# Kernel optimization log

Hardware: AMD Instinct MI355X
Metric: run time of the kernel (lower is better)

## Reference

```python
import math
import jax, jax.numpy as jnp
import numpy as np

N_HEAD = 16
N_KV_HEAD = 4
HEAD_DIM = 64
EPS = 1e-6  # flax nnx.RMSNorm default epsilon
NEG_INF = -1000000000.0


def apply_rotary_emb(x, cos, sin):
    # x: (B,T,H,hd); cos/sin broadcast to (B,T,H,hd//2)
    d = x.shape[3] // 2
    x1, x2 = x[..., :d], x[..., d:]
    y1 = x1 * cos + x2 * sin
    y2 = x1 * -sin + x2 * cos
    return jnp.concatenate([y1, y2], axis=3).astype(x.dtype)


def rmsnorm_noscale(x):
    # flax nnx.RMSNorm(use_scale=False): x * rsqrt(mean(x^2) + eps)
    ms = jnp.mean(jnp.square(x), axis=-1, keepdims=True)
    return x * jax.lax.rsqrt(ms + EPS)


def setup_inputs() -> dict:
    key = jax.random.key(0)
    ks = jax.random.split(key, 7)
    B, T, C = 2, 2048, 1024
    sc = 1.0 / math.sqrt(C)
    x = jax.random.normal(ks[0], (B, T, C), jnp.float32)
    # realistic rotary tables
    pos = jnp.arange(T, dtype=jnp.float32)
    inv_freq = 1.0 / (10000.0 ** (jnp.arange(0, HEAD_DIM // 2, dtype=jnp.float32) / (HEAD_DIM // 2)))
    ang = pos[:, None] * inv_freq[None, :]  # (T, hd/2)
    cos = jnp.cos(ang)[None, :, None, :]
    sin = jnp.sin(ang)[None, :, None, :]
    Wq = jax.random.normal(ks[1], (C, N_HEAD * HEAD_DIM), jnp.float32) * sc
    Wk = jax.random.normal(ks[2], (C, N_KV_HEAD * HEAD_DIM), jnp.float32) * sc
    Wv = jax.random.normal(ks[3], (C, N_KV_HEAD * HEAD_DIM), jnp.float32) * sc
    Wo = jax.random.normal(ks[4], (C, C), jnp.float32) * sc
    return {"x": x, "cos": cos, "sin": sin, "Wq": Wq, "Wk": Wk, "Wv": Wv, "Wo": Wo}


def reference(x, cos, sin, Wq, Wk, Wv, Wo):
    B, T, C = x.shape
    q = (x @ Wq).reshape(B, T, N_HEAD, HEAD_DIM)
    k = (x @ Wk).reshape(B, T, N_KV_HEAD, HEAD_DIM)
    v = (x @ Wv).reshape(B, T, N_KV_HEAD, HEAD_DIM)
    q = rmsnorm_noscale(apply_rotary_emb(q, cos, sin))
    k = rmsnorm_noscale(apply_rotary_emb(k, cos, sin))
    q = jnp.transpose(q, (0, 2, 1, 3))  # (B,H,T,hd)
    k = jnp.transpose(k, (0, 2, 1, 3))  # (B,KV,T,hd)
    v = jnp.transpose(v, (0, 2, 1, 3))
    n_rep = N_HEAD // N_KV_HEAD
    k = jnp.repeat(k, n_rep, axis=1)
    v = jnp.repeat(v, n_rep, axis=1)
    scale = 1.0 / math.sqrt(HEAD_DIM)
    logits = jnp.einsum('bhtd,bhsd->bhts', q, k) * scale
    causal = jnp.where(jnp.tril(jnp.ones((T, T), dtype=jnp.bool_)), 0.0, NEG_INF)
    logits = logits + causal
    w = jax.nn.softmax(logits, axis=-1)
    y = jnp.einsum('bhts,bhsd->bhtd', w, v)
    y = jnp.transpose(y, (0, 2, 1, 3)).reshape(B, T, C)
    return y @ Wo
```

## Files before the change

kernel.cpp:

```cpp
#include <hip/hip_runtime.h>
#include <hip/hip_bf16.h>
#include <math.h>

#define EPS 1e-6f
#define LOG2E 1.44269504088896340736f

typedef __attribute__((ext_vector_type(8))) short short8;
typedef __attribute__((ext_vector_type(4))) short short4v;
typedef __attribute__((ext_vector_type(4))) float f32x4;

static __device__ __forceinline__ short f2bf(float x) {
    unsigned u = __builtin_bit_cast(unsigned, x);
    u += 0x7fffu + ((u >> 16) & 1u);
    return (short)(u >> 16);
}
static __device__ __forceinline__ float bf2f(short s) {
    unsigned u = ((unsigned)(unsigned short)s) << 16;
    return __builtin_bit_cast(float, u);
}

typedef __attribute__((address_space(1))) const void gvoid_t;
typedef __attribute__((address_space(3))) void lvoid_t;
static __device__ __forceinline__ void gload_lds16(const void* g, void* l) {
    __builtin_amdgcn_global_load_lds((gvoid_t*)g, (lvoid_t*)l, 16, 0, 0);
}

__global__ __launch_bounds__(256) void prep_inputs(
    const float* __restrict__ x, const float* __restrict__ Wq,
    const float* __restrict__ Wk, const float* __restrict__ Wv,
    const float* __restrict__ Wo, short* __restrict__ x16,
    short* __restrict__ WT, short* __restrict__ WoT, int n8) {
    if ((int)blockIdx.x < 2048) {
        const int i = blockIdx.x * 256 + threadIdx.x;
        if (i >= n8) return;
        const float4 a = reinterpret_cast<const float4*>(x)[2 * i];
        const float4 b = reinterpret_cast<const float4*>(x)[2 * i + 1];
        short8 o;
        o[0] = f2bf(a.x); o[1] = f2bf(a.y); o[2] = f2bf(a.z); o[3] = f2bf(a.w);
        o[4] = f2bf(b.x); o[5] = f2bf(b.y); o[6] = f2bf(b.z); o[7] = f2bf(b.w);
        reinterpret_cast<short8*>(x16)[i] = o;
        return;
    }
    __shared__ short tl[64][65];
    int t = blockIdx.x - 2048;
    const float* src; short* dst; int N, nx;
    if (t < 256)      { src = Wq; dst = WT;                N = 1024; nx = 16; }
    else if (t < 320) { src = Wk; dst = WT + 1024 * 1024;  N = 256;  nx = 4;  t -= 256; }
    else if (t < 384) { src = Wv; dst = WT + 1280 * 1024;  N = 256;  nx = 4;  t -= 320; }
    else              { src = Wo; dst = WoT;               N = 1024; nx = 16; t -= 384; }
    const int n0 = (t % nx) * 64, k0 = (t / nx) * 64;
    const int tid = threadIdx.x;

    #pragma unroll
    for (int i = 0; i < 4; ++i) {
        const int kr = (tid >> 4) + i * 16;
        const int c4 = (tid & 15) * 4;
        const float4 v = *reinterpret_cast<const float4*>(
            &src[(size_t)(k0 + kr) * N + n0 + c4]);
        tl[kr][c4 + 0] = f2bf(v.x);
        tl[kr][c4 + 1] = f2bf(v.y);
        tl[kr][c4 + 2] = f2bf(v.z);
        tl[kr][c4 + 3] = f2bf(v.w);
    }
    __syncthreads();

    const int nr  = tid >> 2;
    const int kc0 = (tid & 3) * 16;
    short tmp[16];
    #pragma unroll
    for (int j = 0; j < 16; ++j) tmp[j] = tl[kc0 + j][nr];
    short8* outp = reinterpret_cast<short8*>(&dst[(size_t)(n0 + nr) * 1024 + k0 + kc0]);
    outp[0] = *reinterpret_cast<short8*>(&tmp[0]);
    outp[1] = *reinterpret_cast<short8*>(&tmp[8]);
}

template <int OB>
__global__ __launch_bounds__(256) void gemm_bf16(const short* __restrict__ A,
                                                 const short* __restrict__ BT,
                                                 float* __restrict__ Cf,
                                                 short* __restrict__ Cb,
                                                 int M, int N, int K) {
    __shared__ short As[2][128 * 64];
    __shared__ short Bs[2][64 * 64];

    const int tid  = threadIdx.x;
    const int lane = tid & 63;
    const int w    = tid >> 6;
    const int lq = lane & 15, lh = lane >> 4;
    const int wm = w >> 1,   wn = w & 1;
    const size_t arow0 = (size_t)blockIdx.x * 128;
    const size_t brow0 = (size_t)blockIdx.y * 64;

    const int sr  = lane >> 3;
    const int sc  = lane & 7;
    const int scg = sc ^ sr;

    f32x4 acc[4][2];
    #pragma unroll
    for (int mi = 0; mi < 4; ++mi)
        #pragma unroll
        for (int ni = 0; ni < 2; ++ni) acc[mi][ni] = (f32x4){0.f, 0.f, 0.f, 0.f};

    const int NT = K >> 6;

    auto STAGE = [&](int u, int k0) {
        #pragma unroll
        for (int i = 0; i < 4; ++i) {
            const int rg = w * 4 + i;
            gload_lds16(A + (arow0 + rg * 8 + sr) * K + k0 + scg * 8,
                        &As[u][rg * 8 * 64]);
        }
        #pragma unroll
        for (int i = 0; i < 2; ++i) {
            const int rg = w * 2 + i;
            gload_lds16(BT + (brow0 + rg * 8 + sr) * K + k0 + scg * 8,
                        &Bs[u][rg * 8 * 64]);
        }
    };

    STAGE(0, 0);
    __syncthreads();
    int cur = 0;

    for (int t = 0; t < NT; ++t) {
        if (t + 1 < NT) STAGE(cur ^ 1, (t + 1) << 6);

        #pragma unroll
        for (int dk = 0; dk < 2; ++dk) {
            short8 af[4], bf[2];
            #pragma unroll
            for (int mi = 0; mi < 4; ++mi) {
                const int r = wm * 64 + mi * 16 + lq;
                af[mi] = *reinterpret_cast<const short8*>(
                    &As[cur][r * 64 + (((dk * 4 + lh) ^ (lq & 7)) * 8)]);
            }
            #pragma unroll
            for (int ni = 0; ni < 2; ++ni) {
                const int r = wn * 32 + ni * 16 + lq;
                bf[ni] = *reinterpret_cast<const short8*>(
                    &Bs[cur][r * 64 + (((dk * 4 + lh) ^ (lq & 7)) * 8)]);
            }
            __builtin_amdgcn_s_setprio(1);
            #pragma unroll
            for (int mi = 0; mi < 4; ++mi)
                #pragma unroll
                for (int ni = 0; ni < 2; ++ni)
                    acc[mi][ni] = __builtin_amdgcn_mfma_f32_16x16x32_bf16(
                        af[mi], bf[ni], acc[mi][ni], 0, 0, 0);
            __builtin_amdgcn_s_setprio(0);
        }

        __syncthreads();
        cur ^= 1;
    }

    #pragma unroll
    for (int mi = 0; mi < 4; ++mi) {
        const size_t row = arow0 + wm * 64 + mi * 16 + lh * 4;
        #pragma unroll
        for (int ni = 0; ni < 2; ++ni) {
            const size_t col = brow0 + wn * 32 + ni * 16 + lq;
            #pragma unroll
            for (int i = 0; i < 4; ++i) {
                if (OB) Cb[(row + i) * N + col] = f2bf(acc[mi][ni][i]);
                else    Cf[(row + i) * N + col] = acc[mi][ni][i];
            }
        }
    }
}

__global__ __launch_bounds__(256) void rope_v_prep(
    const short* __restrict__ qkv16, const float* __restrict__ cosb,
    const float* __restrict__ sinb, short* __restrict__ q16,
    short* __restrict__ k16, short* __restrict__ vT, int B, int T) {
    const int NR = B * T * 5;
    if ((int)blockIdx.x < NR) {
        const int lane = threadIdx.x & 63;
        const int wid  = threadIdx.x >> 6;
        const int row  = blockIdx.x * 4 + wid;
        const int bt = row / 20;
        const int h  = row % 20;
        const int b  = bt / T, t = bt % T;

        const short* src = (h < 16) ? qkv16 + (size_t)bt * 1536 + h * 64
                                    : qkv16 + (size_t)bt * 1536 + 1024 + (h - 16) * 64;

        const int j = lane & 31;
        const float x1 = bf2f(src[j]);
        const float x2 = bf2f(src[j + 32]);
        const float c = cosb[t * 32 + j];
        const float s = sinb[t * 32 + j];
        float y = (lane < 32) ? (x1 * c + x2 * s) : (x2 * c - x1 * s);

        float ss = y * y;
        #pragma unroll
        for (int m = 1; m < 64; m <<= 1) ss += __shfl_xor(ss, m);
        const float r = rsqrtf(ss * (1.0f / 64.0f) + EPS);

        if (h < 16)
            q16[((size_t)(b * 16 + h) * T + t) * 64 + lane] = f2bf(y * r * (0.125f * LOG2E));
        else
            k16[((size_t)(b * 4 + (h - 16)) * T + t) * 64 + lane] = f2bf(y * r);
        return;
    }

    __shared__ short tl[64][65];
    const int vt = blockIdx.x - NR;
    const int ntile = T >> 6;
    const int b   = vt / (4 * ntile);
    const int kvh = (vt / ntile) & 3;
    const int t0  = (vt % ntile) * 64;
    const int tid = threadIdx.x;

    #pragma unroll
    for (int i = 0; i < 4; ++i) {
        const int tr = (tid >> 4) + i * 16;
        const int d4 = (tid & 15) * 4;
        const short4v v4 = *reinterpret_cast<const short4v*>(
            &qkv16[(size_t)(b * T + t0 + tr) * 1536 + 1280 + kvh * 64 + d4]);
        tl[tr][d4 + 0] = v4[0];
        tl[tr][d4 + 1] = v4[1];
        tl[tr][d4 + 2] = v4[2];
        tl[tr][d4 + 3] = v4[3];
    }
    __syncthreads();

    const int dim = tid >> 2;
    const int tq  = (tid & 3) * 16;
    const int hi  = (tq >> 4) & 1;
    const int a32 = tq & 32;
    short tmp[16];
    #pragma unroll
    for (int j2 = 0; j2 < 16; ++j2) tmp[j2] = tl[tq + j2][dim];
    short* orow = &vT[((size_t)(b * 4 + kvh) * 64 + dim) * T + t0];
    #pragma unroll
    for (int g = 0; g < 4; ++g) {
        *reinterpret_cast<short4v*>(orow + a32 + g * 8 + hi * 4) =
            *reinterpret_cast<short4v*>(&tmp[g * 4]);
    }
}

__global__ __launch_bounds__(128) void attn_mfma(
    const short* __restrict__ q16, const short* __restrict__ k16,
    const short* __restrict__ vT16, short* __restrict__ att16, int B, int T) {
    __shared__ short Kt[64 * 64];
    __shared__ short Vt[64 * 64];

    const int tid  = threadIdx.x;
    const int lane = tid & 63;
    const int w    = tid >> 6;
    const int lq   = lane & 15;
    const int lh   = lane >> 4;

    const int idx = blockIdx.x;
    const int g   = idx & 7;
    const int j   = idx >> 3;
    const int b   = g >> 2;
    const int hk  = g & 3;
    const int qs  = (T >> 5) - 1 - (j >> 2);
    const int h   = hk * 4 + (j & 3);
    const int t0w = qs * 32 + w * 16;
    const int nt  = (qs >> 1) + 1;
    const bool evenq = !(qs & 1);

    const short* qrow = q16 + ((size_t)(b * 16 + h) * T + t0w + lq) * 64;
    const short8 qf0 = *reinterpret_cast<const short8*>(qrow + lh * 8);
    const short8 qf1 = *reinterpret_cast<const short8*>(qrow + 32 + lh * 8);

    const short* kgbase = k16 + (size_t)(b * 4 + hk) * T * 64;
    const short* vgbase = vT16 + (size_t)(b * 4 + hk) * 64 * T;

    const int sr  = lane >> 3;
    const int sc  = lane & 7;
    const int scg = sc ^ sr;

    short8 ones;
    #pragma unroll
    for (int i = 0; i < 8; ++i) ones[i] = (short)0x3F80;

    f32x4 yacc[4];
    #pragma unroll
    for (int dt = 0; dt < 4; ++dt) yacc[dt] = (f32x4){0.f, 0.f, 0.f, 0.f};
    f32x4 lacc = (f32x4){0.f, 0.f, 0.f, 0.f};

    for (int ti = 0; ti < nt; ++ti) {
        const int s0 = ti * 64;
        const bool last = (ti == nt - 1);
        const int kmax = (last && evenq) ? 2 : 4;
        __syncthreads();
        #pragma unroll
        for (int p2 = 0; p2 < 4; ++p2) {
            const int r = w * 32 + p2 * 8 + sr;
            gload_lds16(kgbase + (size_t)(s0 + r) * 64 + scg * 8,
                        &Kt[(w * 32 + p2 * 8) * 64]);
            gload_lds16(vgbase + (size_t)r * T + s0 + scg * 8,
                        &Vt[(w * 32 + p2 * 8) * 64]);
        }
        __syncthreads();

        f32x4 st[4];
        __builtin_amdgcn_s_setprio(1);
        #pragma unroll
        for (int ks = 0; ks < 4; ++ks) if (ks < kmax) {
            f32x4 a1 = (f32x4){0.f, 0.f, 0.f, 0.f};
            #pragma unroll
            for (int dk = 0; dk < 2; ++dk) {
                const short8 kfr = *reinterpret_cast<const short8*>(
                    (char*)Kt + (ks * 16 + lq) * 128 +
                    (((dk * 4 + lh) ^ (lq & 7)) * 16));
                a1 = __builtin_amdgcn_mfma_f32_16x16x32_bf16(
                    kfr, dk ? qf1 : qf0, a1, 0, 0, 0);
            }
            st[ks] = a1;
        }
        __builtin_amdgcn_s_setprio(0);

        if (last) {
            const int rloc = (qs & 1) * 32 + w * 16 + lq;
            #pragma unroll
            for (int ks = 0; ks < 4; ++ks) if (ks < kmax)
                #pragma unroll
                for (int i2 = 0; i2 < 4; ++i2)
                    if (ks * 16 + lh * 4 + i2 > rloc)
                        st[ks][i2] = -1e30f;
        }

        union { short8 s8; __hip_bfloat162 h2[4]; } pf[2];
        #pragma unroll
        for (int ks2 = 0; ks2 < 2; ++ks2) if (ks2 * 2 < kmax) {
            #pragma unroll
            for (int ks = 2 * ks2; ks < 2 * ks2 + 2; ++ks)
                #pragma unroll
                for (int i2 = 0; i2 < 4; ++i2)
                    st[ks][i2] = exp2f(st[ks][i2]);
            pf[ks2].h2[0] = __float22bfloat162_rn(float2{st[2 * ks2][0], st[2 * ks2][1]});
            pf[ks2].h2[1] = __float22bfloat162_rn(float2{st[2 * ks2][2], st[2 * ks2][3]});
            pf[ks2].h2[2] = __float22bfloat162_rn(float2{st[2 * ks2 + 1][0], st[2 * ks2 + 1][1]});
            pf[ks2].h2[3] = __float22bfloat162_rn(float2{st[2 * ks2 + 1][2], st[2 * ks2 + 1][3]});
        }

        __builtin_amdgcn_s_setprio(1);
        #pragma unroll
        for (int ks2 = 0; ks2 < 2; ++ks2) if (ks2 * 2 < kmax)
            lacc = __builtin_amdgcn_mfma_f32_16x16x32_bf16(ones, pf[ks2].s8, lacc, 0, 0, 0);
        #pragma unroll
        for (int dt = 0; dt < 4; ++dt) {
            const int rb = (dt * 16 + lq) * 128;
            const int sw = lq & 7;
            #pragma unroll
            for (int ks2 = 0; ks2 < 2; ++ks2) if (ks2 * 2 < kmax) {
                const short8 vf = *reinterpret_cast<const short8*>(
                    (const char*)Vt + rb + (((ks2 * 4 + lh) ^ sw) * 16));
                yacc[dt] = __builtin_amdgcn_mfma_f32_16x16x32_bf16(
                    vf, pf[ks2].s8, yacc[dt], 0, 0, 0);
            }
        }
        __builtin_amdgcn_s_setprio(0);
    }

    const float inv = 1.f / lacc[0];
    short* orow = att16 + (((size_t)b * T + t0w + lq) * 16 + h) * 64;
    #pragma unroll
    for (int dt = 0; dt < 4; ++dt) {
        short4v o;
        o[0] = f2bf(yacc[dt][0] * inv);
        o[1] = f2bf(yacc[dt][1] * inv);
        o[2] = f2bf(yacc[dt][2] * inv);
        o[3] = f2bf(yacc[dt][3] * inv);
        *reinterpret_cast<short4v*>(orow + dt * 16 + lh * 4) = o;
    }
}

extern "C" void kernel_launch(void* const* d_in, const int* in_sizes, int n_in,
                              void* d_out, int out_size, void* d_ws, size_t ws_size,
                              hipStream_t stream) {
    const float* x    = (const float*)d_in[0];
    const float* cosb = (const float*)d_in[1];
    const float* sinb = (const float*)d_in[2];
    const float* Wq   = (const float*)d_in[3];
    const float* Wk   = (const float*)d_in[4];
    const float* Wv   = (const float*)d_in[5];
    const float* Wo   = (const float*)d_in[6];
    float* out = (float*)d_out;

    const int B = 2, T = 2048;
    const int M = B * T;
    const size_t MB = 1 << 20;

    char* wsb = (char*)d_ws;
    short* qkv16 = (short*)(wsb);
    short* att16 = (short*)(wsb);
    short* x16   = (short*)(wsb + 24 * MB);
    short* q16   = (short*)(wsb + 24 * MB);
    short* WT    = (short*)(wsb + 32 * MB);
    short* k16   = (short*)(wsb + 32 * MB);
    short* vT16  = (short*)(wsb + 34 * MB);
    short* WoT   = (short*)(wsb + 36 * MB);

    prep_inputs<<<2048 + 640, 256, 0, stream>>>(x, Wq, Wk, Wv, Wo,
                                                x16, WT, WoT, M * 1024 / 8);

    gemm_bf16<1><<<dim3(M / 128, 1536 / 64), 256, 0, stream>>>(
        x16, WT, nullptr, qkv16, M, 1536, 1024);

    rope_v_prep<<<B * T * 5 + (T / 64) * 4 * B, 256, 0, stream>>>(
        qkv16, cosb, sinb, q16, k16, vT16, B, T);

    attn_mfma<<<dim3((T / 32) * 16 * B), 128, 0, stream>>>(q16, k16, vT16, att16, B, T);

    gemm_bf16<0><<<dim3(M / 128, 1024 / 64), 256, 0, stream>>>(
        att16, WoT, out, nullptr, M, 1024, 1024);
}
```

Baseline: 113.2 us.

## Fuse RoPE, RMSNorm and V transpose into QKV GEMM epilogue

The separate rope_v_prep kernel is removed. The QKV projection GEMM now stages its fp32 accumulator tile in shared memory and, per 64-column head block, applies rotary embedding, RMSNorm and scaling for Q/K, or transposes V, then writes the attention-ready layouts directly. This drops a kernel launch and the bf16 qkv intermediate round trip through global memory, and Q/K are normalised from fp32 rather than from rounded bf16 values. In exchange the GEMM epilogue gets longer, with a serial 32-row loop per wave doing shuffle reductions. The shared buffers are merged into one array so the epilogue can reuse them, and the workspace layout is adjusted.

```diff
diff --git a/kernel.cpp b/kernel.cpp
--- a/kernel.cpp
+++ b/kernel.cpp
@@ -74,15 +74,14 @@
     outp[1] = *reinterpret_cast<short8*>(&tmp[8]);
 }
 
-template <int OB>
-__global__ __launch_bounds__(256) void gemm_bf16(const short* __restrict__ A,
-                                                 const short* __restrict__ BT,
-                                                 float* __restrict__ Cf,
-                                                 short* __restrict__ Cb,
-                                                 int M, int N, int K) {
-    __shared__ short As[2][128 * 64];
-    __shared__ short Bs[2][64 * 64];
-
+__global__ __launch_bounds__(256) void gemm_qkv_fused(
+    const short* __restrict__ A, const short* __restrict__ BT,
+    const float* __restrict__ cosb, const float* __restrict__ sinb,
+    short* __restrict__ q16, short* __restrict__ k16, short* __restrict__ vT,
+    int B, int T) {
+    __shared__ short smem[2][(128 + 64) * 64];
+
+    const int K = 1024;
     const int tid  = threadIdx.x;
     const int lane = tid & 63;
     const int w    = tid >> 6;
@@ -104,17 +103,19 @@
     const int NT = K >> 6;
 
     auto STAGE = [&](int u, int k0) {
+        short* As = smem[u];
+        short* Bs = smem[u] + 128 * 64;
         #pragma unroll
         for (int i = 0; i < 4; ++i) {
             const int rg = w * 4 + i;
             gload_lds16(A + (arow0 + rg * 8 + sr) * K + k0 + scg * 8,
-                        &As[u][rg * 8 * 64]);
+                        &As[rg * 8 * 64]);
         }
         #pragma unroll
         for (int i = 0; i < 2; ++i) {
             const int rg = w * 2 + i;
             gload_lds16(BT + (brow0 + rg * 8 + sr) * K + k0 + scg * 8,
-                        &Bs[u][rg * 8 * 64]);
+                        &Bs[rg * 8 * 64]);
         }
     };
 
@@ -124,6 +125,8 @@
 
     for (int t = 0; t < NT; ++t) {
         if (t + 1 < NT) STAGE(cur ^ 1, (t + 1) << 6);
+        const short* As = smem[cur];
+        const short* Bs = smem[cur] + 128 * 64;
 
         #pragma unroll
         for (int dk = 0; dk < 2; ++dk) {
@@ -132,13 +135,13 @@
             for (int mi = 0; mi < 4; ++mi) {
                 const int r = wm * 64 + mi * 16 + lq;
                 af[mi] = *reinterpret_cast<const short8*>(
-                    &As[cur][r * 64 + (((dk * 4 + lh) ^ (lq & 7)) * 8)]);
+                    &As[r * 64 + (((dk * 4 + lh) ^ (lq & 7)) * 8)]);
             }
             #pragma unroll
             for (int ni = 0; ni < 2; ++ni) {
                 const int r = wn * 32 + ni * 16 + lq;
                 bf[ni] = *reinterpret_cast<const short8*>(
-                    &Bs[cur][r * 64 + (((dk * 4 + lh) ^ (lq & 7)) * 8)]);
+                    &Bs[r * 64 + (((dk * 4 + lh) ^ (lq & 7)) * 8)]);
             }
             __builtin_amdgcn_s_setprio(1);
             #pragma unroll
@@ -154,6 +157,147 @@
         cur ^= 1;
     }
 
+    float* fl = (float*)smem;
+    #pragma unroll
+    for (int mi = 0; mi < 4; ++mi) {
+        const int row = wm * 64 + mi * 16 + lh * 4;
+        #pragma unroll
+        for (int ni = 0; ni < 2; ++ni) {
+            const int col = wn * 32 + ni * 16 + lq;
+            #pragma unroll
+            for (int i = 0; i < 4; ++i)
+                fl[(row + i) * 66 + col] = acc[mi][ni][i];
+        }
+    }
+    __syncthreads();
+
+    const int by = blockIdx.y;
+    const int b  = (int)(arow0 / T);
+    const int t0 = (int)(arow0 % T);
+
+    if (by < 20) {
+        const int j = lane & 31;
+        for (int rr = 0; rr < 32; ++rr) {
+            const int row = w * 32 + rr;
+            const int t   = t0 + row;
+            const float x1 = fl[row * 66 + j];
+            const float x2 = fl[row * 66 + 32 + j];
+            const float c = cosb[t * 32 + j];
+            const float s = sinb[t * 32 + j];
+            float y = (lane < 32) ? (x1 * c + x2 * s) : (x2 * c - x1 * s);
+            float ss = y * y;
+            #pragma unroll
+            for (int m = 1; m < 64; m <<= 1) ss += __shfl_xor(ss, m);
+            const float r = rsqrtf(ss * (1.0f / 64.0f) + EPS);
+            if (by < 16)
+                q16[((size_t)(b * 16 + by) * T + t) * 64 + lane] =
+                    f2bf(y * r * (0.125f * LOG2E));
+            else
+                k16[((size_t)(b * 4 + (by - 16)) * T + t) * 64 + lane] =
+                    f2bf(y * r);
+        }
+    } else {
+        const int kvh = by - 20;
+        const int dim = tid >> 2;
+        const int tq  = (tid & 3) * 16;
+        const int hi  = (tq >> 4) & 1;
+        const int a32 = tq & 32;
+        short* orow = vT + ((size_t)(b * 4 + kvh) * 64 + dim) * T + t0;
+        #pragma unroll
+        for (int th = 0; th < 2; ++th) {
+            short tmp[16];
+            #pragma unroll
+            for (int j2 = 0; j2 < 16; ++j2)
+                tmp[j2] = f2bf(fl[(th * 64 + tq + j2) * 66 + dim]);
+            #pragma unroll
+            for (int g = 0; g < 4; ++g)
+                *reinterpret_cast<short4v*>(orow + th * 64 + a32 + g * 8 + hi * 4) =
+                    *reinterpret_cast<short4v*>(&tmp[g * 4]);
+        }
+    }
+}
+
+__global__ __launch_bounds__(256) void gemm_wo(const short* __restrict__ A,
+                                               const short* __restrict__ BT,
+                                               float* __restrict__ C,
+                                               int M, int N, int K) {
+    __shared__ short smem[2][(128 + 64) * 64];
+
+    const int tid  = threadIdx.x;
+    const int lane = tid & 63;
+    const int w    = tid >> 6;
+    const int lq = lane & 15, lh = lane >> 4;
+    const int wm = w >> 1,   wn = w & 1;
+    const size_t arow0 = (size_t)blockIdx.x * 128;
+    const size_t brow0 = (size_t)blockIdx.y * 64;
+
+    const int sr  = lane >> 3;
+    const int sc  = lane & 7;
+    const int scg = sc ^ sr;
+
+    f32x4 acc[4][2];
+    #pragma unroll
+    for (int mi = 0; mi < 4; ++mi)
+        #pragma unroll
+        for (int ni = 0; ni < 2; ++ni) acc[mi][ni] = (f32x4){0.f, 0.f, 0.f, 0.f};
+
+    const int NT = K >> 6;
+
+    auto STAGE = [&](int u, int k0) {
+        short* As = smem[u];
+        short* Bs = smem[u] + 128 * 64;
+        #pragma unroll
+        for (int i = 0; i < 4; ++i) {
+            const int rg = w * 4 + i;
+            gload_lds16(A + (arow0 + rg * 8 + sr) * K + k0 + scg * 8,
+                        &As[rg * 8 * 64]);
+        }
+        #pragma unroll
+        for (int i = 0; i < 2; ++i) {
+            const int rg = w * 2 + i;
+            gload_lds16(BT + (brow0 + rg * 8 + sr) * K + k0 + scg * 8,
+                        &Bs[rg * 8 * 64]);
+        }
+    };
+
+    STAGE(0, 0);
+    __syncthreads();
+    int cur = 0;
+
+    for (int t = 0; t < NT; ++t) {
+        if (t + 1 < NT) STAGE(cur ^ 1, (t + 1) << 6);
+        const short* As = smem[cur];
+        const short* Bs = smem[cur] + 128 * 64;
+
+        #pragma unroll
+        for (int dk = 0; dk < 2; ++dk) {
+            short8 af[4], bf[2];
+            #pragma unroll
+            for (int mi = 0; mi < 4; ++mi) {
+                const int r = wm * 64 + mi * 16 + lq;
+                af[mi] = *reinterpret_cast<const short8*>(
+                    &As[r * 64 + (((dk * 4 + lh) ^ (lq & 7)) * 8)]);
+            }
+            #pragma unroll
+            for (int ni = 0; ni < 2; ++ni) {
+                const int r = wn * 32 + ni * 16 + lq;
+                bf[ni] = *reinterpret_cast<const short8*>(
+                    &Bs[r * 64 + (((dk * 4 + lh) ^ (lq & 7)) * 8)]);
+            }
+            __builtin_amdgcn_s_setprio(1);
+            #pragma unroll
+            for (int mi = 0; mi < 4; ++mi)
+                #pragma unroll
+                for (int ni = 0; ni < 2; ++ni)
+                    acc[mi][ni] = __builtin_amdgcn_mfma_f32_16x16x32_bf16(
+                        af[mi], bf[ni], acc[mi][ni], 0, 0, 0);
+            __builtin_amdgcn_s_setprio(0);
+        }
+
+        __syncthreads();
+        cur ^= 1;
+    }
+
     #pragma unroll
     for (int mi = 0; mi < 4; ++mi) {
         const size_t row = arow0 + wm * 64 + mi * 16 + lh * 4;
@@ -161,82 +305,9 @@
         for (int ni = 0; ni < 2; ++ni) {
             const size_t col = brow0 + wn * 32 + ni * 16 + lq;
             #pragma unroll
-            for (int i = 0; i < 4; ++i) {
-                if (OB) Cb[(row + i) * N + col] = f2bf(acc[mi][ni][i]);
-                else    Cf[(row + i) * N + col] = acc[mi][ni][i];
-            }
-        }
-    }
-}
-
-__global__ __launch_bounds__(256) void rope_v_prep(
-    const short* __restrict__ qkv16, const float* __restrict__ cosb,
-    const float* __restrict__ sinb, short* __restrict__ q16,
-    short* __restrict__ k16, short* __restrict__ vT, int B, int T) {
-    const int NR = B * T * 5;
-    if ((int)blockIdx.x < NR) {
-        const int lane = threadIdx.x & 63;
-        const int wid  = threadIdx.x >> 6;
-        const int row  = blockIdx.x * 4 + wid;
-        const int bt = row / 20;
-        const int h  = row % 20;
-        const int b  = bt / T, t = bt % T;
-
-        const short* src = (h < 16) ? qkv16 + (size_t)bt * 1536 + h * 64
-                                    : qkv16 + (size_t)bt * 1536 + 1024 + (h - 16) * 64;
-
-        const int j = lane & 31;
-        const float x1 = bf2f(src[j]);
-        const float x2 = bf2f(src[j + 32]);
-        const float c = cosb[t * 32 + j];
-        const float s = sinb[t * 32 + j];
-        float y = (lane < 32) ? (x1 * c + x2 * s) : (x2 * c - x1 * s);
-
-        float ss = y * y;
-        #pragma unroll
-        for (int m = 1; m < 64; m <<= 1) ss += __shfl_xor(ss, m);
-        const float r = rsqrtf(ss * (1.0f / 64.0f) + EPS);
-
-        if (h < 16)
-            q16[((size_t)(b * 16 + h) * T + t) * 64 + lane] = f2bf(y * r * (0.125f * LOG2E));
-        else
-            k16[((size_t)(b * 4 + (h - 16)) * T + t) * 64 + lane] = f2bf(y * r);
-        return;
-    }
-
-    __shared__ short tl[64][65];
-    const int vt = blockIdx.x - NR;
-    const int ntile = T >> 6;
-    const int b   = vt / (4 * ntile);
-    const int kvh = (vt / ntile) & 3;
-    const int t0  = (vt % ntile) * 64;
-    const int tid = threadIdx.x;
-
-    #pragma unroll
-    for (int i = 0; i < 4; ++i) {
-        const int tr = (tid >> 4) + i * 16;
-        const int d4 = (tid & 15) * 4;
-        const short4v v4 = *reinterpret_cast<const short4v*>(
-            &qkv16[(size_t)(b * T + t0 + tr) * 1536 + 1280 + kvh * 64 + d4]);
-        tl[tr][d4 + 0] = v4[0];
-        tl[tr][d4 + 1] = v4[1];
-        tl[tr][d4 + 2] = v4[2];
-        tl[tr][d4 + 3] = v4[3];
-    }
-    __syncthreads();
-
-    const int dim = tid >> 2;
-    const int tq  = (tid & 3) * 16;
-    const int hi  = (tq >> 4) & 1;
-    const int a32 = tq & 32;
-    short tmp[16];
-    #pragma unroll
-    for (int j2 = 0; j2 < 16; ++j2) tmp[j2] = tl[tq + j2][dim];
-    short* orow = &vT[((size_t)(b * 4 + kvh) * 64 + dim) * T + t0];
-    #pragma unroll
-    for (int g = 0; g < 4; ++g) {
-        *reinterpret_cast<short4v*>(orow + a32 + g * 8 + hi * 4) =
-            *reinterpret_cast<short4v*>(&tmp[g * 4]);
+            for (int i = 0; i < 4; ++i)
+                C[(row + i) * N + col] = acc[mi][ni][i];
+        }
     }
 }
 
@@ -388,26 +459,22 @@
     const size_t MB = 1 << 20;
 
     char* wsb = (char*)d_ws;
-    short* qkv16 = (short*)(wsb);
     short* att16 = (short*)(wsb);
+    short* q16   = (short*)(wsb + 8 * MB);
+    short* k16   = (short*)(wsb + 16 * MB);
+    short* vT16  = (short*)(wsb + 18 * MB);
     short* x16   = (short*)(wsb + 24 * MB);
-    short* q16   = (short*)(wsb + 24 * MB);
     short* WT    = (short*)(wsb + 32 * MB);
-    short* k16   = (short*)(wsb + 32 * MB);
-    short* vT16  = (short*)(wsb + 34 * MB);
     short* WoT   = (short*)(wsb + 36 * MB);
 
     prep_inputs<<<2048 + 640, 256, 0, stream>>>(x, Wq, Wk, Wv, Wo,
                                                 x16, WT, WoT, M * 1024 / 8);
 
-    gemm_bf16<1><<<dim3(M / 128, 1536 / 64), 256, 0, stream>>>(
-        x16, WT, nullptr, qkv16, M, 1536, 1024);
-
-    rope_v_prep<<<B * T * 5 + (T / 64) * 4 * B, 256, 0, stream>>>(
-        qkv16, cosb, sinb, q16, k16, vT16, B, T);
+    gemm_qkv_fused<<<dim3(M / 128, 1536 / 64), 256, 0, stream>>>(
+        x16, WT, cosb, sinb, q16, k16, vT16, B, T);
 
     attn_mfma<<<dim3((T / 32) * 16 * B), 128, 0, stream>>>(q16, k16, vT16, att16, B, T);
 
-    gemm_bf16<0><<<dim3(M / 128, 1024 / 64), 256, 0, stream>>>(
-        att16, WoT, out, nullptr, M, 1024, 1024);
-}
+    gemm_wo<<<dim3(M / 128, 1024 / 64), 256, 0, stream>>>(
+        att16, WoT, out, M, 1024, 1024);
+}
```

Result: faster. 102.6 us (-9.4%).
